# Optimization experiments

Hardware: AMD Instinct MI355X
Metric: run time of the kernel (lower is better)

The kernel has to match this reference:

```python
import jax, jax.numpy as jnp
import numpy as np


def setup_inputs() -> dict:
    key = jax.random.key(0)
    ks = jax.random.split(key, 6)
    B, H, W, C = 4, 64, 64, 256
    D = 256 // 4  # inter_channel // 4
    return {
        "g": jax.random.normal(ks[0], (B, H, W, C), dtype=jnp.float32),
        "x": jax.random.normal(ks[1], (B, H, W, C), dtype=jnp.float32),
        "x_query": jax.random.normal(ks[2], (B, H, W, D), dtype=jnp.float32),
        "phi_g": jax.random.normal(ks[3], (B, H, W, D), dtype=jnp.float32),
        "x_value": jax.random.normal(ks[4], (B, H, W, C), dtype=jnp.float32),
        "k": jax.random.normal(ks[5], (1,), dtype=jnp.float32),
    }


def reference(g, x, x_query, phi_g, x_value, k):
    B, H, W, C = x.shape
    D = x_query.shape[-1]
    HW = H * W
    q = x_query.reshape(B, HW, D)
    pg = phi_g.reshape(B, HW, D)
    v = x_value.reshape(B, HW, C)
    # scale[b,i,j] = sum_d phi_g[b,i,d] * x_query[b,j,d]  -> (B, HW, HW)
    scale = jnp.einsum("bid,bjd->bij", pg, q)
    soft = jax.nn.softmax(scale, axis=-1)
    # scaled_value[b,i,c] = sum_j soft[b,i,j] * v[b,j,c]
    sv = jnp.einsum("bij,bjc->bic", soft, v).reshape(B, H, W, C)
    layero = k * sv + x
    return jnp.concatenate([layero, g], axis=3)
```

## Files before the change

kernel.cpp:

```cpp
#include <hip/hip_runtime.h>

#define N_  4096
#define D_  64
#define C_  256

typedef short bf16x8 __attribute__((ext_vector_type(8)));
typedef float f32x4  __attribute__((ext_vector_type(4)));

__device__ __forceinline__ unsigned short f2bf(float f) {
    union { float f; unsigned int i; } v; v.f = f;
    unsigned int r = v.i + 0x7fffu + ((v.i >> 16) & 1u);
    return (unsigned short)(r >> 16);
}

__global__ void prepass_kernel(const float* __restrict__ xq,
                               const float* __restrict__ pg,
                               const float* __restrict__ xv,
                               unsigned short* __restrict__ qbf,
                               unsigned short* __restrict__ pgbf,
                               unsigned short* __restrict__ vt2) {
    const int bid = blockIdx.x;
    const int t   = threadIdx.x;
    if (bid < 512) {
        const float* src = (bid < 256) ? xq : pg;
        unsigned short* dst = (bid < 256) ? qbf : pgbf;
        const int base = (bid & 255) * 1024 + t;
#pragma unroll
        for (int it = 0; it < 4; ++it) {
            const int i = base + it * 256;
            float4 v = ((const float4*)src)[i];
            ushort4 o;
            o.x = f2bf(v.x); o.y = f2bf(v.y); o.z = f2bf(v.z); o.w = f2bf(v.w);
            ((ushort4*)dst)[i] = o;
        }
        return;
    }
    const int lane = t & 63;
    const int w    = t >> 6;
    const int l15  = lane & 15;
    const int quad = lane >> 4;
    const int f    = (bid - 512) * 4 + w;
    const int b    = f >> 11;
    const int jt   = (f >> 6) & 31;
    const int cb   = (f >> 2) & 15;
    const int ks   = f & 3;
    const int c    = cb * 16 + l15;
    const int jb   = jt * 128 + ks * 32 + quad * 8;
    const float* src = xv + ((size_t)b * N_ + jb) * C_ + c;
    float v0 = src[0 * C_], v1 = src[1 * C_], v2 = src[2 * C_], v3 = src[3 * C_];
    float v4 = src[4 * C_], v5 = src[5 * C_], v6 = src[6 * C_], v7 = src[7 * C_];
    uint4 o;
    o.x = (unsigned)f2bf(v0) | ((unsigned)f2bf(v1) << 16);
    o.y = (unsigned)f2bf(v2) | ((unsigned)f2bf(v3) << 16);
    o.z = (unsigned)f2bf(v4) | ((unsigned)f2bf(v5) << 16);
    o.w = (unsigned)f2bf(v6) | ((unsigned)f2bf(v7) << 16);
    *(uint4*)(vt2 + (size_t)f * 512 + lane * 8) = o;
}

__global__ __launch_bounds__(512, 2) void attn_main(
    const float* __restrict__ g,  const float* __restrict__ x,
    const float* __restrict__ kk, float* __restrict__ out,
    const unsigned short* __restrict__ qbf,
    const unsigned short* __restrict__ pgbf,
    const unsigned short* __restrict__ vt2)
{
    __shared__ unsigned short p_lds[2][64][132];
    __shared__ float s_l[64];

    const int t    = threadIdx.x;
    const int lane = t & 63;
    const int w    = t >> 6;
    const int l15  = lane & 15;
    const int quad = lane >> 4;

    const int bid = blockIdx.x;
    const int b   = bid & 3;
    const int rg  = bid >> 2;
    const int i0  = rg * 64;
    const size_t rowbase = (size_t)b * N_ + i0;

    const int wsj = w;
    const int mh  = w >> 2;
    const int ctq = w & 3;

    if (t < 64) s_l[t] = 0.f;

#pragma unroll
    for (int it = 0; it < 8; ++it) {
        const int row = it * 8 + w;
        const int c4  = lane * 4;
        const float4 gv = *(const float4*)(g + (rowbase + row) * C_ + c4);
        *(float4*)(out + (rowbase + row) * (2 * C_) + C_ + c4) = gv;
    }

    bf16x8 pgf[4][2];
#pragma unroll
    for (int mt = 0; mt < 4; ++mt)
#pragma unroll
        for (int ks = 0; ks < 2; ++ks)
            pgf[mt][ks] = *(const bf16x8*)(pgbf +
                (rowbase + mt * 16 + l15) * D_ + ks * 32 + quad * 8);

    f32x4 oacc[2][4];
#pragma unroll
    for (int mtl = 0; mtl < 2; ++mtl)
#pragma unroll
        for (int ct = 0; ct < 4; ++ct) oacc[mtl][ct] = (f32x4){0.f, 0.f, 0.f, 0.f};
    float ls[4][4];
#pragma unroll
    for (int mt = 0; mt < 4; ++mt)
#pragma unroll
        for (int r = 0; r < 4; ++r) ls[mt][r] = 0.f;

    const unsigned short* qb  = qbf + (size_t)b * N_ * D_;
    const unsigned short* vtb = vt2 + (size_t)b * N_ * C_;

    bf16x8 qf[2];
#pragma unroll
    for (int ks = 0; ks < 2; ++ks)
        qf[ks] = *(const bf16x8*)(qb + (size_t)(wsj * 16 + l15) * D_ + ks * 32 + quad * 8);

    __syncthreads();

    for (int jt = 0; jt < 32; ++jt) {
        const int buf = jt & 1;
        const unsigned short* tbase = vtb + (size_t)jt * 32768;

        bf16x8 vfp[4][4];
#pragma unroll
        for (int ks = 0; ks < 4; ++ks)
#pragma unroll
            for (int ct = 0; ct < 4; ++ct)
                vfp[ks][ct] = *(const bf16x8*)(tbase +
                    (size_t)(((ctq * 4 + ct) * 4) + ks) * 512 + lane * 8);

        f32x4 sacc[4];
#pragma unroll
        for (int mt = 0; mt < 4; ++mt) sacc[mt] = (f32x4){0.f, 0.f, 0.f, 0.f};
#pragma unroll
        for (int ks = 0; ks < 2; ++ks)
#pragma unroll
            for (int mt = 0; mt < 4; ++mt)
                sacc[mt] = __builtin_amdgcn_mfma_f32_16x16x32_bf16(pgf[mt][ks], qf[ks], sacc[mt], 0, 0, 0);

#pragma unroll
        for (int mt = 0; mt < 4; ++mt)
#pragma unroll
            for (int r = 0; r < 4; ++r) {
                const float p = __expf(sacc[mt][r]);
                ls[mt][r] += p;
                p_lds[buf][mt * 16 + quad * 4 + r][wsj * 16 + l15] = f2bf(p);
            }
        __syncthreads();

        if (jt < 31) {
            const int jn = (jt + 1) * 128;
#pragma unroll
            for (int ks = 0; ks < 2; ++ks)
                qf[ks] = *(const bf16x8*)(qb +
                    (size_t)(jn + wsj * 16 + l15) * D_ + ks * 32 + quad * 8);
        }

#pragma unroll
        for (int ks = 0; ks < 4; ++ks) {
            union { bf16x8 f; uint2 u2[2]; } pa[2];
#pragma unroll
            for (int mtl = 0; mtl < 2; ++mtl) {
                const unsigned short* prow =
                    &p_lds[buf][(mh * 2 + mtl) * 16 + l15][ks * 32 + quad * 8];
                pa[mtl].u2[0] = *(const uint2*)prow;
                pa[mtl].u2[1] = *(const uint2*)(prow + 4);
            }
#pragma unroll
            for (int ct = 0; ct < 4; ++ct) {
                oacc[0][ct] = __builtin_amdgcn_mfma_f32_16x16x32_bf16(pa[0].f, vfp[ks][ct], oacc[0][ct], 0, 0, 0);
                oacc[1][ct] = __builtin_amdgcn_mfma_f32_16x16x32_bf16(pa[1].f, vfp[ks][ct], oacc[1][ct], 0, 0, 0);
            }
        }
    }

#pragma unroll
    for (int mt = 0; mt < 4; ++mt)
#pragma unroll
        for (int r = 0; r < 4; ++r) {
            float s = ls[mt][r];
            s += __shfl_xor(s, 1); s += __shfl_xor(s, 2);
            s += __shfl_xor(s, 4); s += __shfl_xor(s, 8);
            if (l15 == 0) atomicAdd(&s_l[mt * 16 + quad * 4 + r], s);
        }
    __syncthreads();

    const float kval = kk[0];
#pragma unroll
    for (int mtl = 0; mtl < 2; ++mtl) {
        const int mt = mh * 2 + mtl;
#pragma unroll
        for (int r = 0; r < 4; ++r) {
            const int m = mt * 16 + quad * 4 + r;
            const float linv = 1.f / s_l[m];
            const size_t row = rowbase + m;
#pragma unroll
            for (int ct = 0; ct < 4; ++ct) {
                const int c = ctq * 64 + ct * 16 + l15;
                out[row * (2 * C_) + c] = kval * (oacc[mtl][ct][r] * linv) + x[row * C_ + c];
            }
        }
    }
}

#define ROWS 4
#define FNT  256
__global__ __launch_bounds__(FNT, 2) void attn_fallback(
    const float* __restrict__ g, const float* __restrict__ x,
    const float* __restrict__ xq, const float* __restrict__ pg,
    const float* __restrict__ xv, const float* __restrict__ kk,
    float* __restrict__ out)
{
    __shared__ __align__(16) float s_pg[ROWS][D_];
    __shared__ __align__(16) float s_sc[N_ * ROWS];
    __shared__ float s_rmax[4][ROWS];
    __shared__ float s_rsum[4][ROWS];

    const int t = threadIdx.x, lane = t & 63, w = t >> 6, blk = blockIdx.x;
    const int b = blk >> 10, i0 = (blk & 1023) * ROWS;
    const size_t rowbase = (size_t)b * N_ + i0;
    {
        const int r = t >> 6, cc = (t & 63) * 4;
        const float4 gv = *(const float4*)(g + (rowbase + r) * C_ + cc);
        *(float4*)(out + (rowbase + r) * (2 * C_) + C_ + cc) = gv;
    }
    { const int r = t >> 6, d = t & 63; s_pg[r][d] = pg[(rowbase + r) * D_ + d]; }
    __syncthreads();
    const float* qb = xq + (size_t)b * N_ * D_;
    float lmax[ROWS];
#pragma unroll
    for (int r = 0; r < ROWS; ++r) lmax[r] = -1e30f;
    for (int jj = 0; jj < N_ / FNT; ++jj) {
        const int j = t + jj * FNT;
        const float4* q4p = (const float4*)(qb + (size_t)j * D_);
        float s[ROWS] = {0.f, 0.f, 0.f, 0.f};
#pragma unroll
        for (int u = 0; u < D_ / 8; ++u) {
            const float4 qa = q4p[u * 2], qc = q4p[u * 2 + 1];
#pragma unroll
            for (int r = 0; r < ROWS; ++r) {
                const float4 pa = *(const float4*)&s_pg[r][u * 8];
                const float4 pb = *(const float4*)&s_pg[r][u * 8 + 4];
                s[r] += qa.x * pa.x + qa.y * pa.y + qa.z * pa.z + qa.w * pa.w
                      + qc.x * pb.x + qc.y * pb.y + qc.z * pb.z + qc.w * pb.w;
            }
        }
        *(float4*)&s_sc[j * ROWS] = make_float4(s[0], s[1], s[2], s[3]);
#pragma unroll
        for (int r = 0; r < ROWS; ++r) lmax[r] = fmaxf(lmax[r], s[r]);
    }
#pragma unroll
    for (int r = 0; r < ROWS; ++r) {
        float m = lmax[r];
        for (int o = 32; o > 0; o >>= 1) m = fmaxf(m, __shfl_down(m, o));
        if (lane == 0) s_rmax[w][r] = m;
    }
    __syncthreads();
    float bmax[ROWS];
#pragma unroll
    for (int r = 0; r < ROWS; ++r)
        bmax[r] = fmaxf(fmaxf(s_rmax[0][r], s_rmax[1][r]), fmaxf(s_rmax[2][r], s_rmax[3][r]));
    float lsum[ROWS] = {0.f, 0.f, 0.f, 0.f};
    for (int jj = 0; jj < N_ / FNT; ++jj) {
        const int j = t + jj * FNT;
        float4 s4 = *(const float4*)&s_sc[j * ROWS];
        s4.x = __expf(s4.x - bmax[0]); s4.y = __expf(s4.y - bmax[1]);
        s4.z = __expf(s4.z - bmax[2]); s4.w = __expf(s4.w - bmax[3]);
        *(float4*)&s_sc[j * ROWS] = s4;
        lsum[0] += s4.x; lsum[1] += s4.y; lsum[2] += s4.z; lsum[3] += s4.w;
    }
#pragma unroll
    for (int r = 0; r < ROWS; ++r) {
        float sm = lsum[r];
        for (int o = 32; o > 0; o >>= 1) sm += __shfl_down(sm, o);
        if (lane == 0) s_rsum[w][r] = sm;
    }
    __syncthreads();
    float rinv[ROWS];
#pragma unroll
    for (int r = 0; r < ROWS; ++r)
        rinv[r] = 1.f / (s_rsum[0][r] + s_rsum[1][r] + s_rsum[2][r] + s_rsum[3][r]);
    const int jg = lane >> 4;
    const int c0 = (w * 16 + (lane & 15)) * 4;
    const float* vb = xv + (size_t)b * N_ * C_;
    float acc[ROWS][4];
#pragma unroll
    for (int r = 0; r < ROWS; ++r)
#pragma unroll
        for (int q = 0; q < 4; ++q) acc[r][q] = 0.f;
#pragma unroll 4
    for (int jj = 0; jj < N_ / 4; ++jj) {
        const int j = jj * 4 + jg;
        const float4 p4 = *(const float4*)&s_sc[j * ROWS];
        const float4 v4 = *(const float4*)(vb + (size_t)j * C_ + c0);
        acc[0][0] += p4.x * v4.x; acc[0][1] += p4.x * v4.y; acc[0][2] += p4.x * v4.z; acc[0][3] += p4.x * v4.w;
        acc[1][0] += p4.y * v4.x; acc[1][1] += p4.y * v4.y; acc[1][2] += p4.y * v4.z; acc[1][3] += p4.y * v4.w;
        acc[2][0] += p4.z * v4.x; acc[2][1] += p4.z * v4.y; acc[2][2] += p4.z * v4.z; acc[2][3] += p4.z * v4.w;
        acc[3][0] += p4.w * v4.x; acc[3][1] += p4.w * v4.y; acc[3][2] += p4.w * v4.z; acc[3][3] += p4.w * v4.w;
    }
#pragma unroll
    for (int r = 0; r < ROWS; ++r)
#pragma unroll
        for (int q = 0; q < 4; ++q) {
            acc[r][q] += __shfl_xor(acc[r][q], 16);
            acc[r][q] += __shfl_xor(acc[r][q], 32);
        }
    const float kval = kk[0];
    if (lane < 16) {
        const int c = (w * 16 + lane) * 4;
#pragma unroll
        for (int r = 0; r < ROWS; ++r) {
            const float4 xv4 = *(const float4*)(x + (rowbase + r) * C_ + c);
            float4 ov;
            ov.x = kval * (acc[r][0] * rinv[r]) + xv4.x;
            ov.y = kval * (acc[r][1] * rinv[r]) + xv4.y;
            ov.z = kval * (acc[r][2] * rinv[r]) + xv4.z;
            ov.w = kval * (acc[r][3] * rinv[r]) + xv4.w;
            *(float4*)(out + (rowbase + r) * (2 * C_) + c) = ov;
        }
    }
}

extern "C" void kernel_launch(void* const* d_in, const int* in_sizes, int n_in,
                              void* d_out, int out_size, void* d_ws, size_t ws_size,
                              hipStream_t stream) {
    const float* g  = (const float*)d_in[0];
    const float* x  = (const float*)d_in[1];
    const float* xq = (const float*)d_in[2];
    const float* pg = (const float*)d_in[3];
    const float* xv = (const float*)d_in[4];
    const float* kk = (const float*)d_in[5];
    float* out = (float*)d_out;

    const int B = in_sizes[0] / (N_ * C_);
    const size_t qn = (size_t)B * N_ * D_;
    const size_t vn = (size_t)B * N_ * C_;
    const size_t need = (2 * qn + vn) * sizeof(unsigned short);

    if (ws_size < need) {
        attn_fallback<<<dim3(B * (N_ / ROWS)), FNT, 0, stream>>>(g, x, xq, pg, xv, kk, out);
        return;
    }

    unsigned short* qbf  = (unsigned short*)d_ws;
    unsigned short* pgbf = qbf + qn;
    unsigned short* vt2  = pgbf + qn;

    prepass_kernel<<<dim3(512 + B * 512), 256, 0, stream>>>(xq, pg, xv, qbf, pgbf, vt2);
    attn_main<<<dim3(B * (N_ / 64)), 512, 0, stream>>>(g, x, kk, out, qbf, pgbf, vt2);
}
```

Measured before the change: 173.3 us.

## Fuse bf16 prepass into attention kernel via grid-wide atomic barrier

Merges the bf16 conversion and V transpose prepass into the main attention kernel. A global atomic counter acts as a grid barrier, so each block converts its share before the attention phase. The V transpose now goes through LDS staging to make global reads coalesced. The output split also changes: each wave now owns all 64 rows and 32 columns instead of 32 rows by 64 columns, which changes register use and LDS reads. The fused kernel saves one launch and its gap, but it adds a memset and relies on all 256 blocks being co-resident, otherwise the spin barrier deadlocks.

```diff
diff --git a/kernel.cpp b/kernel.cpp
--- a/kernel.cpp
+++ b/kernel.cpp
@@ -12,59 +12,21 @@
     unsigned int r = v.i + 0x7fffu + ((v.i >> 16) & 1u);
     return (unsigned short)(r >> 16);
 }
-
-__global__ void prepass_kernel(const float* __restrict__ xq,
-                               const float* __restrict__ pg,
-                               const float* __restrict__ xv,
-                               unsigned short* __restrict__ qbf,
-                               unsigned short* __restrict__ pgbf,
-                               unsigned short* __restrict__ vt2) {
-    const int bid = blockIdx.x;
-    const int t   = threadIdx.x;
-    if (bid < 512) {
-        const float* src = (bid < 256) ? xq : pg;
-        unsigned short* dst = (bid < 256) ? qbf : pgbf;
-        const int base = (bid & 255) * 1024 + t;
-#pragma unroll
-        for (int it = 0; it < 4; ++it) {
-            const int i = base + it * 256;
-            float4 v = ((const float4*)src)[i];
-            ushort4 o;
-            o.x = f2bf(v.x); o.y = f2bf(v.y); o.z = f2bf(v.z); o.w = f2bf(v.w);
-            ((ushort4*)dst)[i] = o;
-        }
-        return;
-    }
-    const int lane = t & 63;
-    const int w    = t >> 6;
-    const int l15  = lane & 15;
-    const int quad = lane >> 4;
-    const int f    = (bid - 512) * 4 + w;
-    const int b    = f >> 11;
-    const int jt   = (f >> 6) & 31;
-    const int cb   = (f >> 2) & 15;
-    const int ks   = f & 3;
-    const int c    = cb * 16 + l15;
-    const int jb   = jt * 128 + ks * 32 + quad * 8;
-    const float* src = xv + ((size_t)b * N_ + jb) * C_ + c;
-    float v0 = src[0 * C_], v1 = src[1 * C_], v2 = src[2 * C_], v3 = src[3 * C_];
-    float v4 = src[4 * C_], v5 = src[5 * C_], v6 = src[6 * C_], v7 = src[7 * C_];
-    uint4 o;
-    o.x = (unsigned)f2bf(v0) | ((unsigned)f2bf(v1) << 16);
-    o.y = (unsigned)f2bf(v2) | ((unsigned)f2bf(v3) << 16);
-    o.z = (unsigned)f2bf(v4) | ((unsigned)f2bf(v5) << 16);
-    o.w = (unsigned)f2bf(v6) | ((unsigned)f2bf(v7) << 16);
-    *(uint4*)(vt2 + (size_t)f * 512 + lane * 8) = o;
-}
-
-__global__ __launch_bounds__(512, 2) void attn_main(
+__device__ __forceinline__ unsigned int pk2(float a, float b) {
+    return (unsigned)f2bf(a) | ((unsigned)f2bf(b) << 16);
+}
+
+__global__ __launch_bounds__(512, 2) void attn_fused(
     const float* __restrict__ g,  const float* __restrict__ x,
-    const float* __restrict__ kk, float* __restrict__ out,
-    const unsigned short* __restrict__ qbf,
-    const unsigned short* __restrict__ pgbf,
-    const unsigned short* __restrict__ vt2)
+    const float* __restrict__ xq, const float* __restrict__ pg,
+    const float* __restrict__ xv, const float* __restrict__ kk,
+    float* __restrict__ out,
+    unsigned short* __restrict__ qbf,
+    unsigned short* __restrict__ pgbf,
+    unsigned short* __restrict__ vt2,
+    int* __restrict__ bar, int nblk)
 {
-    __shared__ unsigned short p_lds[2][64][132];
+    __shared__ __align__(16) unsigned short p_lds[2][64][132];
     __shared__ float s_l[64];
 
     const int t    = threadIdx.x;
@@ -72,18 +34,71 @@
     const int w    = t >> 6;
     const int l15  = lane & 15;
     const int quad = lane >> 4;
-
-    const int bid = blockIdx.x;
-    const int b   = bid & 3;
-    const int rg  = bid >> 2;
-    const int i0  = rg * 64;
+    const int bid  = blockIdx.x;
+
+    {
+        const int gtid = bid * 512 + t;
+        const float4* qs = (const float4*)xq;
+        const float4* ps = (const float4*)pg;
+        ushort4* qd = (ushort4*)qbf;
+        ushort4* pd = (ushort4*)pgbf;
+#pragma unroll
+        for (int it = 0; it < 2; ++it) {
+            const int i = gtid + it * 131072;
+            const float4 a = qs[i], c = ps[i];
+            ushort4 oa, oc;
+            oa.x = f2bf(a.x); oa.y = f2bf(a.y); oa.z = f2bf(a.z); oa.w = f2bf(a.w);
+            oc.x = f2bf(c.x); oc.y = f2bf(c.y); oc.z = f2bf(c.z); oc.w = f2bf(c.w);
+            qd[i] = oa; pd[i] = oc;
+        }
+    }
+    {
+        float* vstage = (float*)&p_lds[0][0][0];
+        for (int s = 0; s < 2; ++s) {
+            const int u   = bid * 2 + s;
+            const int ub  = u >> 7, ujt = (u >> 2) & 31, uks = u & 3;
+            const int jb  = ujt * 128 + uks * 32;
+            __syncthreads();
+#pragma unroll
+            for (int it = 0; it < 4; ++it) {
+                const int idx = it * 512 + t;
+                const int row = idx >> 6, c4 = (idx & 63) * 4;
+                *(float4*)&vstage[row * 264 + c4] =
+                    *(const float4*)(xv + ((size_t)ub * N_ + jb + row) * C_ + c4);
+            }
+            __syncthreads();
+#pragma unroll
+            for (int e2 = 0; e2 < 2; ++e2) {
+                const int idx = e2 * 512 + t;
+                const int cb  = idx >> 6, L = idx & 63;
+                const int c   = cb * 16 + (L & 15);
+                const int jr  = (L >> 4) * 8;
+                uint4 o;
+                o.x = pk2(vstage[(jr + 0) * 264 + c], vstage[(jr + 1) * 264 + c]);
+                o.y = pk2(vstage[(jr + 2) * 264 + c], vstage[(jr + 3) * 264 + c]);
+                o.z = pk2(vstage[(jr + 4) * 264 + c], vstage[(jr + 5) * 264 + c]);
+                o.w = pk2(vstage[(jr + 6) * 264 + c], vstage[(jr + 7) * 264 + c]);
+                const size_t f = (((size_t)ub * 32 + ujt) * 16 + cb) * 4 + uks;
+                *(uint4*)(vt2 + f * 512 + (size_t)L * 8) = o;
+            }
+        }
+    }
+    if (t < 64) s_l[t] = 0.f;
+
+    __threadfence();
+    __syncthreads();
+    if (t == 0)
+        __hip_atomic_fetch_add(bar, 1, __ATOMIC_ACQ_REL, __HIP_MEMORY_SCOPE_AGENT);
+    if (lane == 0) {
+        while (__hip_atomic_load(bar, __ATOMIC_ACQUIRE, __HIP_MEMORY_SCOPE_AGENT) < nblk)
+            __builtin_amdgcn_s_sleep(2);
+    }
+    __syncthreads();
+
+    const int b  = bid & 3;
+    const int rg = bid >> 2;
+    const int i0 = rg * 64;
     const size_t rowbase = (size_t)b * N_ + i0;
-
-    const int wsj = w;
-    const int mh  = w >> 2;
-    const int ctq = w & 3;
-
-    if (t < 64) s_l[t] = 0.f;
 
 #pragma unroll
     for (int it = 0; it < 8; ++it) {
@@ -101,11 +116,10 @@
             pgf[mt][ks] = *(const bf16x8*)(pgbf +
                 (rowbase + mt * 16 + l15) * D_ + ks * 32 + quad * 8);
 
-    f32x4 oacc[2][4];
-#pragma unroll
-    for (int mtl = 0; mtl < 2; ++mtl)
-#pragma unroll
-        for (int ct = 0; ct < 4; ++ct) oacc[mtl][ct] = (f32x4){0.f, 0.f, 0.f, 0.f};
+    f32x4 oacc[4][2];
+#pragma unroll
+    for (int mt = 0; mt < 4; ++mt) { oacc[mt][0] = (f32x4){0.f,0.f,0.f,0.f};
+                                     oacc[mt][1] = (f32x4){0.f,0.f,0.f,0.f}; }
     float ls[4][4];
 #pragma unroll
     for (int mt = 0; mt < 4; ++mt)
@@ -118,25 +132,23 @@
     bf16x8 qf[2];
 #pragma unroll
     for (int ks = 0; ks < 2; ++ks)
-        qf[ks] = *(const bf16x8*)(qb + (size_t)(wsj * 16 + l15) * D_ + ks * 32 + quad * 8);
-
-    __syncthreads();
+        qf[ks] = *(const bf16x8*)(qb + (size_t)(w * 16 + l15) * D_ + ks * 32 + quad * 8);
 
     for (int jt = 0; jt < 32; ++jt) {
         const int buf = jt & 1;
         const unsigned short* tbase = vtb + (size_t)jt * 32768;
 
-        bf16x8 vfp[4][4];
+        bf16x8 vf[4][2];
 #pragma unroll
         for (int ks = 0; ks < 4; ++ks)
 #pragma unroll
-            for (int ct = 0; ct < 4; ++ct)
-                vfp[ks][ct] = *(const bf16x8*)(tbase +
-                    (size_t)(((ctq * 4 + ct) * 4) + ks) * 512 + lane * 8);
+            for (int ctl = 0; ctl < 2; ++ctl)
+                vf[ks][ctl] = *(const bf16x8*)(tbase +
+                    (size_t)(((w * 2 + ctl) * 4) + ks) * 512 + lane * 8);
 
         f32x4 sacc[4];
 #pragma unroll
-        for (int mt = 0; mt < 4; ++mt) sacc[mt] = (f32x4){0.f, 0.f, 0.f, 0.f};
+        for (int mt = 0; mt < 4; ++mt) sacc[mt] = (f32x4){0.f,0.f,0.f,0.f};
 #pragma unroll
         for (int ks = 0; ks < 2; ++ks)
 #pragma unroll
@@ -149,7 +161,7 @@
             for (int r = 0; r < 4; ++r) {
                 const float p = __expf(sacc[mt][r]);
                 ls[mt][r] += p;
-                p_lds[buf][mt * 16 + quad * 4 + r][wsj * 16 + l15] = f2bf(p);
+                p_lds[buf][mt * 16 + quad * 4 + r][w * 16 + l15] = f2bf(p);
             }
         __syncthreads();
 
@@ -158,23 +170,22 @@
 #pragma unroll
             for (int ks = 0; ks < 2; ++ks)
                 qf[ks] = *(const bf16x8*)(qb +
-                    (size_t)(jn + wsj * 16 + l15) * D_ + ks * 32 + quad * 8);
+                    (size_t)(jn + w * 16 + l15) * D_ + ks * 32 + quad * 8);
         }
 
 #pragma unroll
         for (int ks = 0; ks < 4; ++ks) {
-            union { bf16x8 f; uint2 u2[2]; } pa[2];
-#pragma unroll
-            for (int mtl = 0; mtl < 2; ++mtl) {
-                const unsigned short* prow =
-                    &p_lds[buf][(mh * 2 + mtl) * 16 + l15][ks * 32 + quad * 8];
-                pa[mtl].u2[0] = *(const uint2*)prow;
-                pa[mtl].u2[1] = *(const uint2*)(prow + 4);
-            }
-#pragma unroll
-            for (int ct = 0; ct < 4; ++ct) {
-                oacc[0][ct] = __builtin_amdgcn_mfma_f32_16x16x32_bf16(pa[0].f, vfp[ks][ct], oacc[0][ct], 0, 0, 0);
-                oacc[1][ct] = __builtin_amdgcn_mfma_f32_16x16x32_bf16(pa[1].f, vfp[ks][ct], oacc[1][ct], 0, 0, 0);
+            union { bf16x8 f; uint2 u2[2]; } pa[4];
+#pragma unroll
+            for (int mt = 0; mt < 4; ++mt) {
+                const unsigned short* prow = &p_lds[buf][mt * 16 + l15][ks * 32 + quad * 8];
+                pa[mt].u2[0] = *(const uint2*)prow;
+                pa[mt].u2[1] = *(const uint2*)(prow + 4);
+            }
+#pragma unroll
+            for (int mt = 0; mt < 4; ++mt) {
+                oacc[mt][0] = __builtin_amdgcn_mfma_f32_16x16x32_bf16(pa[mt].f, vf[ks][0], oacc[mt][0], 0, 0, 0);
+                oacc[mt][1] = __builtin_amdgcn_mfma_f32_16x16x32_bf16(pa[mt].f, vf[ks][1], oacc[mt][1], 0, 0, 0);
             }
         }
     }
@@ -192,20 +203,18 @@
 
     const float kval = kk[0];
 #pragma unroll
-    for (int mtl = 0; mtl < 2; ++mtl) {
-        const int mt = mh * 2 + mtl;
+    for (int mt = 0; mt < 4; ++mt)
 #pragma unroll
         for (int r = 0; r < 4; ++r) {
             const int m = mt * 16 + quad * 4 + r;
             const float linv = 1.f / s_l[m];
             const size_t row = rowbase + m;
 #pragma unroll
-            for (int ct = 0; ct < 4; ++ct) {
-                const int c = ctq * 64 + ct * 16 + l15;
-                out[row * (2 * C_) + c] = kval * (oacc[mtl][ct][r] * linv) + x[row * C_ + c];
-            }
-        }
-    }
+            for (int ctl = 0; ctl < 2; ++ctl) {
+                const int c = w * 32 + ctl * 16 + l15;
+                out[row * (2 * C_) + c] = kval * (oacc[mt][ctl][r] * linv) + x[row * C_ + c];
+            }
+        }
 }
 
 #define ROWS 4
@@ -340,17 +349,20 @@
     const int B = in_sizes[0] / (N_ * C_);
     const size_t qn = (size_t)B * N_ * D_;
     const size_t vn = (size_t)B * N_ * C_;
-    const size_t need = (2 * qn + vn) * sizeof(unsigned short);
-
-    if (ws_size < need) {
+    const size_t need = 64 + (2 * qn + vn) * sizeof(unsigned short);
+
+    if (B != 4 || ws_size < need) {
         attn_fallback<<<dim3(B * (N_ / ROWS)), FNT, 0, stream>>>(g, x, xq, pg, xv, kk, out);
         return;
     }
 
-    unsigned short* qbf  = (unsigned short*)d_ws;
+    int* bar = (int*)d_ws;
+    unsigned short* qbf  = (unsigned short*)((char*)d_ws + 64);
     unsigned short* pgbf = qbf + qn;
     unsigned short* vt2  = pgbf + qn;
 
-    prepass_kernel<<<dim3(512 + B * 512), 256, 0, stream>>>(xq, pg, xv, qbf, pgbf, vt2);
-    attn_main<<<dim3(B * (N_ / 64)), 512, 0, stream>>>(g, x, kk, out, qbf, pgbf, vt2);
-}
+    hipMemsetAsync(d_ws, 0, 64, stream);
+    const int nblk = B * (N_ / 64);
+    attn_fused<<<dim3(nblk), 512, 0, stream>>>(g, x, xq, pg, xv, kk, out,
+                                               qbf, pgbf, vt2, bar, nblk);
+}
```

After: 246.9 us. +42.5%, slower.
